# Kernel optimization log

Measured on AMD Instinct MI355X. Metric: run time of the kernel, lower is better.

Reference implementation:

```python
import jax, jax.numpy as jnp
import numpy as np

DROPOUT_P = 0.5  # pre-softmax dropout prob from __init__
_MASK_KEY = jax.random.key(42)  # fixed key -> deterministic dropout mask


def setup_inputs() -> dict:
    key = jax.random.key(0)
    kq, kk, kv = jax.random.split(key, 3)
    shape = (4, 16, 1024, 64)  # [B, H, S, D]
    Q = jax.random.normal(kq, shape, dtype=jnp.float32)
    K = jax.random.normal(kk, shape, dtype=jnp.float32)
    V = jax.random.normal(kv, shape, dtype=jnp.float32)
    return {"Q": Q, "K": K, "V": V}


def reference(Q, K, V):
    # scores: [B, H, S, S] = Q @ K^T  (no 1/sqrt(d) scaling: scale=False)
    scores = jnp.einsum("bhqd,bhkd->bhqk", Q, K)
    # pre-softmax dropout (train mode, p=0.5), deterministic fixed-key mask
    keep = jax.random.bernoulli(_MASK_KEY, 1.0 - DROPOUT_P, scores.shape)
    scores = jnp.where(keep, scores / (1.0 - DROPOUT_P), 0.0)
    attn = jax.nn.softmax(scores, axis=-1)
    return jnp.einsum("bhqk,bhkd->bhqd", attn, V)
```

## Files before the change

### kernel.cpp

```cpp
#include <hip/hip_runtime.h>
#include <hip/hip_bf16.h>
#include <hip/hip_fp16.h>

typedef _Float16 f16x8 __attribute__((ext_vector_type(8)));
typedef __fp16  h16x2 __attribute__((ext_vector_type(2)));
typedef float f32x4 __attribute__((ext_vector_type(4)));

#define S_LEN 1024
#define DH 64
#define KVB 64
#define NIT 16
#define KROW 72

__device__ __forceinline__ unsigned rotl(unsigned x, unsigned r) {
  return __builtin_amdgcn_alignbit(x, x, 32u - r);
}

__device__ __forceinline__ bool keep_bit(unsigned e) {
  const unsigned ks1 = 42u;
  const unsigned ks2 = 0x1BD11BF0u;
  unsigned x0 = 0u;
  unsigned x1 = e + ks1;
#define TFR(Ra,Rb,Rc,Rd) \
  x0 += x1; x1 = rotl(x1, Ra); x1 ^= x0; \
  x0 += x1; x1 = rotl(x1, Rb); x1 ^= x0; \
  x0 += x1; x1 = rotl(x1, Rc); x1 ^= x0; \
  x0 += x1; x1 = rotl(x1, Rd); x1 ^= x0;
  TFR(13u,15u,26u, 6u)  x0 += ks1; x1 += ks2 + 1u;
  TFR(17u,29u,16u,24u)  x0 += ks2; x1 += 2u;
  TFR(13u,15u,26u, 6u)     x1 += ks1 + 3u;
  TFR(17u,29u,16u,24u)  x0 += ks1; x1 += ks2 + 4u;
  TFR(13u,15u,26u, 6u)  x0 += ks2; x1 += 5u;
#undef TFR
  return ((x0 ^ x1) >> 31) == 0u;
}

__device__ __forceinline__ f16x8 pk8(f32x4 a, f32x4 b) {
  h16x2 p0 = __builtin_amdgcn_cvt_pkrtz(a[0], a[1]);
  h16x2 p1 = __builtin_amdgcn_cvt_pkrtz(a[2], a[3]);
  h16x2 p2 = __builtin_amdgcn_cvt_pkrtz(b[0], b[1]);
  h16x2 p3 = __builtin_amdgcn_cvt_pkrtz(b[2], b[3]);
  f16x8 r;
  r[0]=(_Float16)p0[0]; r[1]=(_Float16)p0[1]; r[2]=(_Float16)p1[0]; r[3]=(_Float16)p1[1];
  r[4]=(_Float16)p2[0]; r[5]=(_Float16)p2[1]; r[6]=(_Float16)p3[0]; r[7]=(_Float16)p3[1];
  return r;
}

__global__ __launch_bounds__(256)
void attn_dropout_kernel(const float* __restrict__ Q, const float* __restrict__ K,
                         const float* __restrict__ V, float* __restrict__ out) {
  __shared__ _Float16 Kl[KVB][KROW];
  __shared__ _Float16 Vt[DH][KROW];
  __shared__ _Float16 Pl[4][16][KROW];

  const unsigned bh   = blockIdx.x >> 4;
  const unsigned q0   = (blockIdx.x & 15u) * 64u;
  const unsigned tid  = threadIdx.x;
  const unsigned w    = tid >> 6;
  const unsigned lane = tid & 63u;
  const unsigned g    = lane >> 4;
  const unsigned ln   = lane & 15u;
  const unsigned qw   = q0 + w * 16u;

  f16x8 Qa0, Qa1;
  {
    const float* Qp = Q + (size_t)(bh * S_LEN + qw + ln) * DH + g * 8;
    f32x4 a = *(const f32x4*)(Qp)      * 2.0f;
    f32x4 b = *(const f32x4*)(Qp + 4)  * 2.0f;
    f32x4 c = *(const f32x4*)(Qp + 32) * 2.0f;
    f32x4 d = *(const f32x4*)(Qp + 36) * 2.0f;
    Qa0 = pk8(a, b);
    Qa1 = pk8(c, d);
  }

  float mrun[4], lrun[4];
  f32x4 accO[4];
#pragma unroll
  for (int r = 0; r < 4; ++r) { mrun[r] = -1e30f; lrun[r] = 0.0f; }
#pragma unroll
  for (int n = 0; n < 4; ++n) accO[n] = (f32x4){0.f, 0.f, 0.f, 0.f};

  const unsigned kk  = tid >> 2;
  const unsigned dgf = (tid & 3u) * 16u;

  f32x4 kr0, kr1, kr2, kr3, vr0, vr1, vr2, vr3;
  {
    const float* Kp = K + (size_t)(bh * S_LEN + kk) * DH + dgf;
    kr0 = *(const f32x4*)(Kp);  kr1 = *(const f32x4*)(Kp + 4);
    kr2 = *(const f32x4*)(Kp + 8); kr3 = *(const f32x4*)(Kp + 12);
    const float* Vp = V + (size_t)(bh * S_LEN + kk) * DH + dgf;
    vr0 = *(const f32x4*)(Vp);  vr1 = *(const f32x4*)(Vp + 4);
    vr2 = *(const f32x4*)(Vp + 8); vr3 = *(const f32x4*)(Vp + 12);
  }

  for (int t = 0; t < NIT; ++t) {
    __syncthreads();
    *(f16x8*)&Kl[kk][dgf]     = pk8(kr0, kr1);
    *(f16x8*)&Kl[kk][dgf + 8] = pk8(kr2, kr3);
#pragma unroll
    for (int i = 0; i < 4; ++i) {
      Vt[dgf +  0 + i][kk] = (_Float16)vr0[i];
      Vt[dgf +  4 + i][kk] = (_Float16)vr1[i];
      Vt[dgf +  8 + i][kk] = (_Float16)vr2[i];
      Vt[dgf + 12 + i][kk] = (_Float16)vr3[i];
    }
    __syncthreads();

    {
      int tn = (t + 1 < NIT) ? t + 1 : NIT - 1;
      const float* Kp = K + (size_t)(bh * S_LEN + tn * KVB + kk) * DH + dgf;
      kr0 = *(const f32x4*)(Kp);  kr1 = *(const f32x4*)(Kp + 4);
      kr2 = *(const f32x4*)(Kp + 8); kr3 = *(const f32x4*)(Kp + 12);
      const float* Vp = V + (size_t)(bh * S_LEN + tn * KVB + kk) * DH + dgf;
      vr0 = *(const f32x4*)(Vp);  vr1 = *(const f32x4*)(Vp + 4);
      vr2 = *(const f32x4*)(Vp + 8); vr3 = *(const f32x4*)(Vp + 12);
    }

    f32x4 sc[4];
#pragma unroll
    for (int nt = 0; nt < 4; ++nt) {
      f16x8 kb0 = *(const f16x8*)&Kl[nt * 16 + ln][g * 8];
      f16x8 kb1 = *(const f16x8*)&Kl[nt * 16 + ln][32 + g * 8];
      f32x4 a = (f32x4){0.f, 0.f, 0.f, 0.f};
      a = __builtin_amdgcn_mfma_f32_16x16x32_f16(Qa0, kb0, a, 0, 0, 0);
      a = __builtin_amdgcn_mfma_f32_16x16x32_f16(Qa1, kb1, a, 0, 0, 0);
      sc[nt] = a;
    }

    float sm[4][4];
#pragma unroll
    for (int nt = 0; nt < 4; ++nt) {
#pragma unroll
      for (int r = 0; r < 4; ++r) {
        unsigned q  = qw + g * 4 + r;
        unsigned kg = (unsigned)t * KVB + nt * 16 + ln;
        unsigned e  = (bh << 20) + (q << 10) + kg;
        sm[nt][r] = keep_bit(e) ? sc[nt][r] : 0.0f;
      }
    }

    float ps[4][4];
#pragma unroll
    for (int r = 0; r < 4; ++r) {
      float mx = fmaxf(fmaxf(sm[0][r], sm[1][r]), fmaxf(sm[2][r], sm[3][r]));
#pragma unroll
      for (int off = 1; off < 16; off <<= 1) mx = fmaxf(mx, __shfl_xor(mx, off));
      float mn  = fmaxf(mrun[r], mx);
      float scl = __expf(mrun[r] - mn);
      mrun[r] = mn;
      float rs = 0.f;
#pragma unroll
      for (int nt = 0; nt < 4; ++nt) {
        float p = __expf(sm[nt][r] - mn);
        ps[nt][r] = p; rs += p;
      }
#pragma unroll
      for (int off = 1; off < 16; off <<= 1) rs += __shfl_xor(rs, off);
      lrun[r] = lrun[r] * scl + rs;
#pragma unroll
      for (int n = 0; n < 4; ++n) accO[n][r] *= scl;
    }

#pragma unroll
    for (int nt = 0; nt < 4; ++nt)
#pragma unroll
      for (int r = 0; r < 4; ++r)
        Pl[w][g * 4 + r][nt * 16 + ln] = (_Float16)ps[nt][r];

    f16x8 Pa0 = *(const f16x8*)&Pl[w][ln][g * 8];
    f16x8 Pa1 = *(const f16x8*)&Pl[w][ln][32 + g * 8];
#pragma unroll
    for (int nd = 0; nd < 4; ++nd) {
      f16x8 vb0 = *(const f16x8*)&Vt[nd * 16 + ln][g * 8];
      f16x8 vb1 = *(const f16x8*)&Vt[nd * 16 + ln][32 + g * 8];
      accO[nd] = __builtin_amdgcn_mfma_f32_16x16x32_f16(Pa0, vb0, accO[nd], 0, 0, 0);
      accO[nd] = __builtin_amdgcn_mfma_f32_16x16x32_f16(Pa1, vb1, accO[nd], 0, 0, 0);
    }
  }

#pragma unroll
  for (int nd = 0; nd < 4; ++nd) {
#pragma unroll
    for (int r = 0; r < 4; ++r) {
      unsigned q = qw + g * 4 + r;
      out[(size_t)(bh * S_LEN + q) * DH + nd * 16 + ln] = accO[nd][r] / lrun[r];
    }
  }
}

extern "C" void kernel_launch(void* const* d_in, const int* in_sizes, int n_in,
                              void* d_out, int out_size, void* d_ws, size_t ws_size,
                              hipStream_t stream) {
  const float* Q = (const float*)d_in[0];
  const float* K = (const float*)d_in[1];
  const float* V = (const float*)d_in[2];
  float* out = (float*)d_out;
  dim3 grid(64 * 16);
  dim3 block(256);
  hipLaunchKernelGGL(attn_dropout_kernel, grid, block, 0, stream, Q, K, V, out);
}
```

Baseline: 248.8 us.

## Use exp2 with folded log2e, lazy max rescale, and deferred row-sum reduction

Folds log2(e) into the Q prescale so the softmax can use exp2 directly. The running max is only updated, along with rescaling of the accumulator and partial sums, when some tile max exceeds it by more than a threshold, checked wave-wide. The per-tile shuffle reduction of the row sum is replaced by per-lane partial sums that are reduced once at the end. This removes most per-tile cross-lane shuffles and rescale multiplies, at the cost of a wave-level branch and bounded exponent growth that relies on the threshold for fp16 and fp32 safety.

```diff
diff --git a/kernel.cpp b/kernel.cpp
--- a/kernel.cpp
+++ b/kernel.cpp
@@ -1,6 +1,7 @@
 #include <hip/hip_runtime.h>
 #include <hip/hip_bf16.h>
 #include <hip/hip_fp16.h>
+#include <math.h>
 
 typedef _Float16 f16x8 __attribute__((ext_vector_type(8)));
 typedef __fp16  h16x2 __attribute__((ext_vector_type(2)));
@@ -11,6 +12,7 @@
 #define KVB 64
 #define NIT 16
 #define KROW 72
+#define THR 11.0f
 
 __device__ __forceinline__ unsigned rotl(unsigned x, unsigned r) {
   return __builtin_amdgcn_alignbit(x, x, 32u - r);
@@ -65,18 +67,19 @@
   f16x8 Qa0, Qa1;
   {
     const float* Qp = Q + (size_t)(bh * S_LEN + qw + ln) * DH + g * 8;
-    f32x4 a = *(const f32x4*)(Qp)      * 2.0f;
-    f32x4 b = *(const f32x4*)(Qp + 4)  * 2.0f;
-    f32x4 c = *(const f32x4*)(Qp + 32) * 2.0f;
-    f32x4 d = *(const f32x4*)(Qp + 36) * 2.0f;
+    const float s = 2.885390082f;
+    f32x4 a = *(const f32x4*)(Qp)      * s;
+    f32x4 b = *(const f32x4*)(Qp + 4)  * s;
+    f32x4 c = *(const f32x4*)(Qp + 32) * s;
+    f32x4 d = *(const f32x4*)(Qp + 36) * s;
     Qa0 = pk8(a, b);
     Qa1 = pk8(c, d);
   }
 
-  float mrun[4], lrun[4];
+  float mrun[4], lpart[4];
   f32x4 accO[4];
 #pragma unroll
-  for (int r = 0; r < 4; ++r) { mrun[r] = -1e30f; lrun[r] = 0.0f; }
+  for (int r = 0; r < 4; ++r) { mrun[r] = -1e30f; lpart[r] = 0.0f; }
 #pragma unroll
   for (int n = 0; n < 4; ++n) accO[n] = (f32x4){0.f, 0.f, 0.f, 0.f};
 
@@ -128,6 +131,9 @@
     }
 
     float sm[4][4];
+    float pmx[4];
+#pragma unroll
+    for (int r = 0; r < 4; ++r) pmx[r] = -1e30f;
 #pragma unroll
     for (int nt = 0; nt < 4; ++nt) {
 #pragma unroll
@@ -135,30 +141,38 @@
         unsigned q  = qw + g * 4 + r;
         unsigned kg = (unsigned)t * KVB + nt * 16 + ln;
         unsigned e  = (bh << 20) + (q << 10) + kg;
-        sm[nt][r] = keep_bit(e) ? sc[nt][r] : 0.0f;
+        float v = keep_bit(e) ? sc[nt][r] : 0.0f;
+        sm[nt][r] = v;
+        pmx[r] = fmaxf(pmx[r], v);
       }
     }
 
+    bool need = (pmx[0] > mrun[0] + THR) | (pmx[1] > mrun[1] + THR) |
+                (pmx[2] > mrun[2] + THR) | (pmx[3] > mrun[3] + THR);
+    if (__any(need)) {
+#pragma unroll
+      for (int r = 0; r < 4; ++r) {
+        float mx = pmx[r];
+#pragma unroll
+        for (int off = 1; off < 16; off <<= 1) mx = fmaxf(mx, __shfl_xor(mx, off));
+        float mn  = fmaxf(mrun[r], mx);
+        float scl = exp2f(mrun[r] - mn);
+        mrun[r] = mn;
+        lpart[r] *= scl;
+#pragma unroll
+        for (int n = 0; n < 4; ++n) accO[n][r] *= scl;
+      }
+    }
+
     float ps[4][4];
 #pragma unroll
-    for (int r = 0; r < 4; ++r) {
-      float mx = fmaxf(fmaxf(sm[0][r], sm[1][r]), fmaxf(sm[2][r], sm[3][r]));
-#pragma unroll
-      for (int off = 1; off < 16; off <<= 1) mx = fmaxf(mx, __shfl_xor(mx, off));
-      float mn  = fmaxf(mrun[r], mx);
-      float scl = __expf(mrun[r] - mn);
-      mrun[r] = mn;
-      float rs = 0.f;
-#pragma unroll
-      for (int nt = 0; nt < 4; ++nt) {
-        float p = __expf(sm[nt][r] - mn);
-        ps[nt][r] = p; rs += p;
+    for (int nt = 0; nt < 4; ++nt) {
+#pragma unroll
+      for (int r = 0; r < 4; ++r) {
+        float p = exp2f(sm[nt][r] - mrun[r]);
+        ps[nt][r] = p;
+        lpart[r] += p;
       }
-#pragma unroll
-      for (int off = 1; off < 16; off <<= 1) rs += __shfl_xor(rs, off);
-      lrun[r] = lrun[r] * scl + rs;
-#pragma unroll
-      for (int n = 0; n < 4; ++n) accO[n][r] *= scl;
     }
 
 #pragma unroll
@@ -178,12 +192,20 @@
     }
   }
 
+  float lf[4];
+#pragma unroll
+  for (int r = 0; r < 4; ++r) {
+    float l = lpart[r];
+#pragma unroll
+    for (int off = 1; off < 16; off <<= 1) l += __shfl_xor(l, off);
+    lf[r] = l;
+  }
 #pragma unroll
   for (int nd = 0; nd < 4; ++nd) {
 #pragma unroll
     for (int r = 0; r < 4; ++r) {
       unsigned q = qw + g * 4 + r;
-      out[(size_t)(bh * S_LEN + q) * DH + nd * 16 + ln] = accO[nd][r] / lrun[r];
+      out[(size_t)(bh * S_LEN + q) * DH + nd * 16 + ln] = accO[nd][r] / lf[r];
     }
   }
 }
```

Measured after the change: 242.2 us. 2.6% less time.
